# Kernel tuning notes

Hardware: AMD Instinct MI355X
Metric: run time of the kernel (lower is better)

## Reference

```python
import jax, jax.numpy as jnp
import numpy as np

NUM_HEAD = 16


def setup_inputs() -> dict:
    key = jax.random.key(0)
    k1, k2, k3 = jax.random.split(key, 3)
    E = 1024
    x = jax.random.normal(k1, (4, 2048, E), dtype=jnp.float32)
    W1 = jax.random.normal(k2, (E, 3 * E), dtype=jnp.float32) * 0.02
    b1 = jnp.zeros((3 * E,), dtype=jnp.float32)
    W2 = jax.random.normal(k3, (E, E), dtype=jnp.float32) * 0.02
    b2 = jnp.zeros((E,), dtype=jnp.float32)
    return {"x": x, "W1": W1, "b1": b1, "W2": W2, "b2": b2}


def reference(x, W1, b1, W2, b2):
    # Fused QKV projection: (n, s, 3E)
    h = x @ W1 + b1
    n, s, _ = h.shape
    # Split into heads FIRST (matches torch reshape), then transpose: (n, H, s, 3*d_head)
    h = h.reshape(n, s, NUM_HEAD, -1).transpose(0, 2, 1, 3)
    # Chunk last dim into q, k, v: each (n, H, s, d_head)
    q, k, v = jnp.split(h, 3, axis=-1)
    dk = jnp.asarray(v.shape[-1], x.dtype) ** 0.5
    # Naive full S x S attention (faithful to source)
    w = jnp.einsum("nhqd,nhkd->nhqk", q, k) / dk
    w = jax.nn.softmax(w, axis=-1)  # dropout1 is identity at eval
    att = jnp.einsum("nhqk,nhkd->nhqd", w, v)
    att = att.transpose(0, 2, 1, 3).reshape(n, s, -1)  # (n, s, E)
    return att @ W2 + b2  # dropout2 identity at eval
```

## Files before the change

### kernel.cpp

```cpp
#include <hip/hip_runtime.h>
#include <math.h>
#include <stdint.h>
#include <stddef.h>


#define SEQ    2048
#define NB     4
#define E_DIM  1024
#define N1     3072
#define M_TOK  8192
#define NHEAD  16
#define DHEAD  64

typedef __attribute__((ext_vector_type(4))) float    floatx4;
typedef __attribute__((ext_vector_type(8))) short    shortx8;
typedef __attribute__((ext_vector_type(4))) unsigned short ushortx4;

#if __has_builtin(__builtin_amdgcn_exp2f)
#define EXP2(x) __builtin_amdgcn_exp2f(x)
#else
#define EXP2(x) __expf((x) * 0.6931471805599453f)
#endif

__device__ __forceinline__ unsigned short f2bf(float f) {
    union { float f; unsigned u; } v; v.f = f;
    unsigned r = (v.u + 0x7FFFu + ((v.u >> 16) & 1u)) >> 16;
    return (unsigned short)r;
}
__device__ __forceinline__ unsigned fbits(float f) {
    union { float f; unsigned u; } v; v.f = f; return v.u;
}
__device__ __forceinline__ float bitsf(unsigned u) {
    union { unsigned u; float f; } v; v.u = u; return v.f;
}

__device__ __forceinline__ void gl_lds16(const void* g, void* l) {
    __builtin_amdgcn_global_load_lds(
        (const __attribute__((address_space(1))) unsigned int*)g,
        (__attribute__((address_space(3))) unsigned int*)l, 16, 0, 0);
}

__global__ __launch_bounds__(256) void cvt_bf16(
    const float* __restrict__ in, unsigned short* __restrict__ out)
{
    const size_t i = ((size_t)blockIdx.x * 256 + threadIdx.x) * 8;
    float4 a = *(const float4*)(in + i);
    float4 b = *(const float4*)(in + i + 4);
    ushortx4 o0 = { f2bf(a.x), f2bf(a.y), f2bf(a.z), f2bf(a.w) };
    ushortx4 o1 = { f2bf(b.x), f2bf(b.y), f2bf(b.z), f2bf(b.w) };
    *(ushortx4*)(out + i)     = o0;
    *(ushortx4*)(out + i + 4) = o1;
}

__global__ __launch_bounds__(256) void cvt_transpose(
    const float* __restrict__ W, unsigned short* __restrict__ Wt, int K, int N)
{
    __shared__ unsigned short tile[32][33];
    const int tx = threadIdx.x, ty = threadIdx.y;
    const int n0 = blockIdx.x * 32, k0 = blockIdx.y * 32;
#pragma unroll
    for (int r = 0; r < 4; ++r) {
        const int k = ty + r * 8;
        tile[tx][k] = f2bf(W[(size_t)(k0 + k) * N + n0 + tx]);
    }
    __syncthreads();
#pragma unroll
    for (int r = 0; r < 4; ++r) {
        const int n = ty + r * 8;
        Wt[(size_t)(n0 + n) * K + k0 + tx] = tile[n][tx];
    }
}

template <bool OUT_BF16, bool FUSE>
__global__ __launch_bounds__(256) void gemm_bf16(
    const short* __restrict__ A, const short* __restrict__ Bt,
    const float* __restrict__ bias, void* __restrict__ Cout,
    unsigned short* __restrict__ Vt,
    int M, int N, int K)
{
    __shared__ short As[128 * 32];
    __shared__ short Bs[128 * 32];

    const int t    = threadIdx.x;
    const int lane = t & 63, w = t >> 6;
    const int quad = lane >> 4, l15 = lane & 15;
    const int bm = blockIdx.y * 128, bn = blockIdx.x * 128;
    const int m0w = (w >> 1) * 64, n0w = (w & 1) * 64;

    const int lrow = lane >> 2;
    const int lcol = (lane & 3) * 8;
    const short* Ag0 = A  + (size_t)(bm + (2 * w + 0) * 16 + lrow) * K + lcol;
    const short* Ag1 = A  + (size_t)(bm + (2 * w + 1) * 16 + lrow) * K + lcol;
    const short* Bg0 = Bt + (size_t)(bn + (2 * w + 0) * 16 + lrow) * K + lcol;
    const short* Bg1 = Bt + (size_t)(bn + (2 * w + 1) * 16 + lrow) * K + lcol;
    short* Al0 = As + (2 * w + 0) * 512;
    short* Al1 = As + (2 * w + 1) * 512;
    short* Bl0 = Bs + (2 * w + 0) * 512;
    short* Bl1 = Bs + (2 * w + 1) * 512;

    floatx4 acc[4][4];
#pragma unroll
    for (int i = 0; i < 4; ++i)
#pragma unroll
        for (int j = 0; j < 4; ++j) acc[i][j] = (floatx4)0.f;

    for (int k0 = 0; k0 < K; k0 += 32) {
        __syncthreads();
        gl_lds16(Ag0, Al0); gl_lds16(Ag1, Al1);
        gl_lds16(Bg0, Bl0); gl_lds16(Bg1, Bl1);
        Ag0 += 32; Ag1 += 32; Bg0 += 32; Bg1 += 32;
        __syncthreads();

        shortx8 af[4], bf[4];
#pragma unroll
        for (int mi = 0; mi < 4; ++mi)
            af[mi] = *(const shortx8*)(As + (m0w + mi * 16 + l15) * 32 + quad * 8);
#pragma unroll
        for (int ni = 0; ni < 4; ++ni)
            bf[ni] = *(const shortx8*)(Bs + (n0w + ni * 16 + l15) * 32 + quad * 8);
#pragma unroll
        for (int mi = 0; mi < 4; ++mi)
#pragma unroll
            for (int ni = 0; ni < 4; ++ni)
                acc[mi][ni] = __builtin_amdgcn_mfma_f32_16x16x32_bf16(
                    af[mi], bf[ni], acc[mi][ni], 0, 0, 0);
    }

    float bv[4];
#pragma unroll
    for (int ni = 0; ni < 4; ++ni) bv[ni] = bias[bn + n0w + ni * 16 + l15];

#pragma unroll
    for (int ni = 0; ni < 4; ++ni) {
        const int col   = bn + n0w + ni * 16 + l15;
        const int cm    = col % 192;
        const int vhead = col / 192;
#pragma unroll
        for (int mi = 0; mi < 4; ++mi) {
            const int row0 = bm + m0w + mi * 16 + quad * 4;
            float v[4];
#pragma unroll
            for (int r = 0; r < 4; ++r) v[r] = acc[mi][ni][r] + bv[ni];
            if (OUT_BF16) {
                if (FUSE && cm < DHEAD) {
#pragma unroll
                    for (int r = 0; r < 4; ++r) v[r] *= 0.18033688011112042f;
                }
                unsigned short* H = (unsigned short*)Cout;
#pragma unroll
                for (int r = 0; r < 4; ++r)
                    H[(size_t)(row0 + r) * N + col] = f2bf(v[r]);
                if (FUSE && cm >= 2 * DHEAD) {
                    const int nb = row0 >> 11;
                    const int s  = row0 & 2047;
                    const int d  = cm - 2 * DHEAD;
                    ushortx4 pk = { f2bf(v[0]), f2bf(v[1]), f2bf(v[2]), f2bf(v[3]) };
                    *(ushortx4*)(Vt + ((size_t)(nb * NHEAD + vhead) * DHEAD + d) * SEQ + s) = pk;
                }
            } else {
                float* C = (float*)Cout;
#pragma unroll
                for (int r = 0; r < 4; ++r)
                    C[(size_t)(row0 + r) * N + col] = v[r];
            }
        }
    }
}

__global__ __launch_bounds__(256, 4) void attn_mfma(
    const short* __restrict__ h, const short* __restrict__ Vt,
    unsigned short* __restrict__ att)
{
    __shared__ short Ks[64 * 64];
    __shared__ short Vs[64 * 64];
    __shared__ short Pl[2][64 * 64];
    __shared__ float Ls2[2][2][64];

    const int t    = threadIdx.x;
    const int lane = t & 63, w = t >> 6;
    const int p    = w >> 1, e = w & 1;
    const int quad = lane >> 4, l15 = lane & 15;
    const int r7   = l15 & 7;
    const int bh = blockIdx.x, n = bh >> 4, head = bh & 15;
    const int q0 = blockIdx.y * 128 + p * 64;

    const short* hQ  = h + (size_t)n * SEQ * N1 + head * (3 * DHEAD);
    const short* hK  = hQ + DHEAD;
    const short* Vtb = Vt + (size_t)bh * DHEAD * SEQ;

    const int srow = t >> 2;
    const int sc0  = (t & 3) * 2;
    const int sk   = srow & 7;
    const short* gK = hK  + (size_t)srow * N1  + sc0 * 8;
    const short* gV = Vtb + (size_t)srow * SEQ + sc0 * 8;
    short* lK0 = Ks + srow * 64 + ((sc0    ) ^ sk) * 8;
    short* lK1 = Ks + srow * 64 + ((sc0 + 1) ^ sk) * 8;
    short* lV0 = Vs + srow * 64 + ((sc0    ) ^ sk) * 8;
    short* lV1 = Vs + srow * 64 + ((sc0 + 1) ^ sk) * 8;

    shortx8 qf[4][2];
#pragma unroll
    for (int qt = 0; qt < 4; ++qt)
#pragma unroll
        for (int kt = 0; kt < 2; ++kt)
            qf[qt][kt] = *(const shortx8*)(hQ + (size_t)(q0 + qt * 16 + l15) * N1
                                           + kt * 32 + quad * 8);

    floatx4 O[4][2];
    float lsum[4];
#pragma unroll
    for (int mi = 0; mi < 4; ++mi) {
        lsum[mi] = 0.f;
#pragma unroll
        for (int nt = 0; nt < 2; ++nt) O[mi][nt] = (floatx4)0.f;
    }

    int4 ka = *(const int4*)gK, kb = *(const int4*)(gK + 8);
    int4 va = *(const int4*)gV, vb = *(const int4*)(gV + 8);

    short* Pp = Pl[p];

    for (int kv0 = 0; kv0 < SEQ; kv0 += 64) {
        __syncthreads();
        *(int4*)lK0 = ka;
        *(int4*)lK1 = kb;
        *(int4*)lV0 = va;
        *(int4*)lV1 = vb;
        __syncthreads();
        if (kv0 + 64 < SEQ) {
            const short* gKn = gK + (size_t)(kv0 + 64) * N1;
            const short* gVn = gV + (kv0 + 64);
            ka = *(const int4*)gKn; kb = *(const int4*)(gKn + 8);
            va = *(const int4*)gVn; vb = *(const int4*)(gVn + 8);
        }

#pragma unroll
        for (int ii = 0; ii < 2; ++ii) {
            const int si = 2 * e + ii;
            const short* krow = Ks + (si * 16 + l15) * 64;
            shortx8 kf0 = *(const shortx8*)(krow + ((quad ^ r7) * 8));
            shortx8 kf1 = *(const shortx8*)(krow + (((quad ^ 4) ^ r7) * 8));
            floatx4 s[4];
#pragma unroll
            for (int qt = 0; qt < 4; ++qt) {
                s[qt] = __builtin_amdgcn_mfma_f32_16x16x32_bf16(
                    kf0, qf[qt][0], (floatx4)0.f, 0, 0, 0);
                s[qt] = __builtin_amdgcn_mfma_f32_16x16x32_bf16(
                    kf1, qf[qt][1], s[qt], 0, 0, 0);
            }
#pragma unroll
            for (int qt = 0; qt < 4; ++qt) {
                const float p0 = EXP2(s[qt][0]);
                const float p1 = EXP2(s[qt][1]);
                const float p2 = EXP2(s[qt][2]);
                const float p3 = EXP2(s[qt][3]);
                const unsigned d01 = __builtin_amdgcn_perm(fbits(p1), fbits(p0), 0x07060302u);
                const unsigned d23 = __builtin_amdgcn_perm(fbits(p3), fbits(p2), 0x07060302u);
                lsum[qt] += bitsf(d01 << 16) + bitsf(d01 & 0xFFFF0000u)
                          + bitsf(d23 << 16) + bitsf(d23 & 0xFFFF0000u);
                uint2 pk = { d01, d23 };
                *(uint2*)(Pp + (qt * 16 + l15) * 64
                          + ((si * 2 + (quad >> 1)) ^ r7) * 8 + (quad & 1) * 4) = pk;
            }
        }
        __syncthreads();

#pragma unroll
        for (int kt2 = 0; kt2 < 2; ++kt2) {
            const int coff = ((kt2 * 4 + quad) ^ r7) * 8;
            shortx8 pf[4], vf[2];
#pragma unroll
            for (int mi = 0; mi < 4; ++mi)
                pf[mi] = *(const shortx8*)(Pp + (mi * 16 + l15) * 64 + coff);
#pragma unroll
            for (int nt = 0; nt < 2; ++nt)
                vf[nt] = *(const shortx8*)(Vs + ((2 * e + nt) * 16 + l15) * 64 + coff);
#pragma unroll
            for (int mi = 0; mi < 4; ++mi)
#pragma unroll
                for (int nt = 0; nt < 2; ++nt)
                    O[mi][nt] = __builtin_amdgcn_mfma_f32_16x16x32_bf16(
                        pf[mi], vf[nt], O[mi][nt], 0, 0, 0);
        }
    }

#pragma unroll
    for (int qt = 0; qt < 4; ++qt) {
        lsum[qt] += __shfl_xor(lsum[qt], 16);
        lsum[qt] += __shfl_xor(lsum[qt], 32);
    }
    if (quad == 0) {
#pragma unroll
        for (int qt = 0; qt < 4; ++qt) Ls2[p][e][qt * 16 + l15] = lsum[qt];
    }
    __syncthreads();

#pragma unroll
    for (int mi = 0; mi < 4; ++mi)
#pragma unroll
        for (int r = 0; r < 4; ++r) {
            const int   ql  = mi * 16 + quad * 4 + r;
            const float inv = 1.f / (Ls2[p][0][ql] + Ls2[p][1][ql]);
            const size_t row = (size_t)n * SEQ + q0 + ql;
#pragma unroll
            for (int nt = 0; nt < 2; ++nt)
                att[row * E_DIM + head * DHEAD + (2 * e + nt) * 16 + l15] =
                    f2bf(O[mi][nt][r] * inv);
        }
}

extern "C" void kernel_launch(void* const* d_in, const int* in_sizes, int n_in,
                              void* d_out, int out_size, void* d_ws, size_t ws_size,
                              hipStream_t stream)
{
    const float* x  = (const float*)d_in[0];
    const float* W1 = (const float*)d_in[1];
    const float* b1 = (const float*)d_in[2];
    const float* W2 = (const float*)d_in[3];
    const float* b2 = (const float*)d_in[4];
    float* out = (float*)d_out;

    char* ws = (char*)d_ws;
    unsigned short* x_bf  = (unsigned short*)(ws);
    unsigned short* W1t   = (unsigned short*)(ws + (16u << 20));
    unsigned short* W2t   = (unsigned short*)(ws + (22u << 20));
    unsigned short* h_bf  = (unsigned short*)(ws + (24u << 20));
    unsigned short* attb  = (unsigned short*)(ws + (72u << 20));
    unsigned short* Vtw   = (unsigned short*)(ws + (88u << 20));

    cvt_bf16<<<dim3((M_TOK * E_DIM) / (256 * 8)), 256, 0, stream>>>(x, x_bf);
    cvt_transpose<<<dim3(N1 / 32, E_DIM / 32), dim3(32, 8), 0, stream>>>(W1, W1t, E_DIM, N1);
    cvt_transpose<<<dim3(E_DIM / 32, E_DIM / 32), dim3(32, 8), 0, stream>>>(W2, W2t, E_DIM, E_DIM);

    gemm_bf16<true, true><<<dim3(N1 / 128, M_TOK / 128), 256, 0, stream>>>(
        (const short*)x_bf, (const short*)W1t, b1, h_bf, Vtw, M_TOK, N1, E_DIM);

    attn_mfma<<<dim3(NB * NHEAD, SEQ / 128), 256, 0, stream>>>(
        (const short*)h_bf, (const short*)Vtw, attb);

    gemm_bf16<false, false><<<dim3(E_DIM / 128, M_TOK / 128), 256, 0, stream>>>(
        (const short*)attb, (const short*)W2t, b2, out, nullptr, M_TOK, E_DIM, E_DIM);
}
```

Baseline: 298.2 us.

## Keep attention probabilities in registers and double-buffer K/V tiles

Restructures the attention kernel so each wave owns 32 query rows and feeds the exponentiated scores straight from MFMA output registers into a 16x16x16 MFMA against V. This removes the P round-trip through shared memory and one barrier per tile. The row sums come from an extra MFMA with a ones vector instead of scalar adds and a cross-wave LDS reduction. K/V tiles are double-buffered in LDS so only one barrier per iteration remains, at the cost of more LDS and more, smaller MFMAs.

```diff
diff --git a/kernel.cpp b/kernel.cpp
--- a/kernel.cpp
+++ b/kernel.cpp
@@ -14,6 +14,7 @@
 
 typedef __attribute__((ext_vector_type(4))) float    floatx4;
 typedef __attribute__((ext_vector_type(8))) short    shortx8;
+typedef __attribute__((ext_vector_type(4))) short    shortx4;
 typedef __attribute__((ext_vector_type(4))) unsigned short ushortx4;
 
 #if __has_builtin(__builtin_amdgcn_exp2f)
@@ -22,6 +23,9 @@
 #define EXP2(x) __expf((x) * 0.6931471805599453f)
 #endif
 
+#define MFMA_K16(a, b, c) \
+    __builtin_amdgcn_mfma_f32_16x16x16bf16_1k((a), (b), (c), 0, 0, 0)
+
 __device__ __forceinline__ unsigned short f2bf(float f) {
     union { float f; unsigned u; } v; v.f = f;
     unsigned r = (v.u + 0x7FFFu + ((v.u >> 16) & 1u)) >> 16;
@@ -29,9 +33,6 @@
 }
 __device__ __forceinline__ unsigned fbits(float f) {
     union { float f; unsigned u; } v; v.f = f; return v.u;
-}
-__device__ __forceinline__ float bitsf(unsigned u) {
-    union { unsigned u; float f; } v; v.u = u; return v.f;
 }
 
 __device__ __forceinline__ void gl_lds16(const void* g, void* l) {
@@ -171,18 +172,15 @@
     const short* __restrict__ h, const short* __restrict__ Vt,
     unsigned short* __restrict__ att)
 {
-    __shared__ short Ks[64 * 64];
-    __shared__ short Vs[64 * 64];
-    __shared__ short Pl[2][64 * 64];
-    __shared__ float Ls2[2][2][64];
+    __shared__ short Ks[2][64 * 64];
+    __shared__ short Vs[2][64 * 64];
 
     const int t    = threadIdx.x;
     const int lane = t & 63, w = t >> 6;
-    const int p    = w >> 1, e = w & 1;
     const int quad = lane >> 4, l15 = lane & 15;
     const int r7   = l15 & 7;
     const int bh = blockIdx.x, n = bh >> 4, head = bh & 15;
-    const int q0 = blockIdx.y * 128 + p * 64;
+    const int q0 = blockIdx.y * 128 + w * 32;
 
     const short* hQ  = h + (size_t)n * SEQ * N1 + head * (3 * DHEAD);
     const short* hK  = hQ + DHEAD;
@@ -193,119 +191,105 @@
     const int sk   = srow & 7;
     const short* gK = hK  + (size_t)srow * N1  + sc0 * 8;
     const short* gV = Vtb + (size_t)srow * SEQ + sc0 * 8;
-    short* lK0 = Ks + srow * 64 + ((sc0    ) ^ sk) * 8;
-    short* lK1 = Ks + srow * 64 + ((sc0 + 1) ^ sk) * 8;
-    short* lV0 = Vs + srow * 64 + ((sc0    ) ^ sk) * 8;
-    short* lV1 = Vs + srow * 64 + ((sc0 + 1) ^ sk) * 8;
-
-    shortx8 qf[4][2];
-#pragma unroll
-    for (int qt = 0; qt < 4; ++qt)
+    const int oL0 = srow * 64 + ((sc0    ) ^ sk) * 8;
+    const int oL1 = srow * 64 + ((sc0 + 1) ^ sk) * 8;
+
+    shortx8 qf[2][2];
+#pragma unroll
+    for (int qt = 0; qt < 2; ++qt)
 #pragma unroll
         for (int kt = 0; kt < 2; ++kt)
             qf[qt][kt] = *(const shortx8*)(hQ + (size_t)(q0 + qt * 16 + l15) * N1
                                            + kt * 32 + quad * 8);
 
-    floatx4 O[4][2];
-    float lsum[4];
-#pragma unroll
-    for (int mi = 0; mi < 4; ++mi) {
-        lsum[mi] = 0.f;
-#pragma unroll
-        for (int nt = 0; nt < 2; ++nt) O[mi][nt] = (floatx4)0.f;
-    }
+    floatx4 O[2][4];
+    floatx4 Osum[2];
+#pragma unroll
+    for (int qt = 0; qt < 2; ++qt) {
+        Osum[qt] = (floatx4)0.f;
+#pragma unroll
+        for (int dt = 0; dt < 4; ++dt) O[qt][dt] = (floatx4)0.f;
+    }
+
+    const shortx4 ones = { (short)0x3F80, (short)0x3F80, (short)0x3F80, (short)0x3F80 };
+
+    const int NT = SEQ / 64;
 
     int4 ka = *(const int4*)gK, kb = *(const int4*)(gK + 8);
     int4 va = *(const int4*)gV, vb = *(const int4*)(gV + 8);
-
-    short* Pp = Pl[p];
-
-    for (int kv0 = 0; kv0 < SEQ; kv0 += 64) {
+    *(int4*)(&Ks[0][oL0]) = ka; *(int4*)(&Ks[0][oL1]) = kb;
+    *(int4*)(&Vs[0][oL0]) = va; *(int4*)(&Vs[0][oL1]) = vb;
+    gK += (size_t)64 * N1; gV += 64;
+
+    for (int it = 0; it < NT; ++it) {
+        const int buf = it & 1;
         __syncthreads();
-        *(int4*)lK0 = ka;
-        *(int4*)lK1 = kb;
-        *(int4*)lV0 = va;
-        *(int4*)lV1 = vb;
-        __syncthreads();
-        if (kv0 + 64 < SEQ) {
-            const short* gKn = gK + (size_t)(kv0 + 64) * N1;
-            const short* gVn = gV + (kv0 + 64);
-            ka = *(const int4*)gKn; kb = *(const int4*)(gKn + 8);
-            va = *(const int4*)gVn; vb = *(const int4*)(gVn + 8);
-        }
-
-#pragma unroll
-        for (int ii = 0; ii < 2; ++ii) {
-            const int si = 2 * e + ii;
-            const short* krow = Ks + (si * 16 + l15) * 64;
+
+        const bool more = (it + 1 < NT);
+        if (more) {
+            ka = *(const int4*)gK; kb = *(const int4*)(gK + 8);
+            va = *(const int4*)gV; vb = *(const int4*)(gV + 8);
+            gK += (size_t)64 * N1; gV += 64;
+        }
+
+        const short* Kb = &Ks[buf][0];
+        const short* Vb = &Vs[buf][0];
+
+#pragma unroll
+        for (int sl = 0; sl < 4; ++sl) {
+            const short* krow = Kb + (sl * 16 + l15) * 64;
             shortx8 kf0 = *(const shortx8*)(krow + ((quad ^ r7) * 8));
             shortx8 kf1 = *(const shortx8*)(krow + (((quad ^ 4) ^ r7) * 8));
-            floatx4 s[4];
-#pragma unroll
-            for (int qt = 0; qt < 4; ++qt) {
-                s[qt] = __builtin_amdgcn_mfma_f32_16x16x32_bf16(
+            shortx4 vf[4];
+#pragma unroll
+            for (int dt = 0; dt < 4; ++dt)
+                vf[dt] = *(const shortx4*)(Vb + (dt * 16 + l15) * 64
+                                           + (((sl * 4 + quad) ^ (r7 << 1)) << 2));
+
+            shortx4 pa[2];
+#pragma unroll
+            for (int qt = 0; qt < 2; ++qt) {
+                floatx4 s = __builtin_amdgcn_mfma_f32_16x16x32_bf16(
                     kf0, qf[qt][0], (floatx4)0.f, 0, 0, 0);
-                s[qt] = __builtin_amdgcn_mfma_f32_16x16x32_bf16(
-                    kf1, qf[qt][1], s[qt], 0, 0, 0);
+                s = __builtin_amdgcn_mfma_f32_16x16x32_bf16(
+                    kf1, qf[qt][1], s, 0, 0, 0);
+                const float p0 = EXP2(s[0]);
+                const float p1 = EXP2(s[1]);
+                const float p2 = EXP2(s[2]);
+                const float p3 = EXP2(s[3]);
+                union { uint2 u; shortx4 v; } cv;
+                cv.u.x = __builtin_amdgcn_perm(fbits(p1), fbits(p0), 0x07060302u);
+                cv.u.y = __builtin_amdgcn_perm(fbits(p3), fbits(p2), 0x07060302u);
+                pa[qt] = cv.v;
             }
-#pragma unroll
-            for (int qt = 0; qt < 4; ++qt) {
-                const float p0 = EXP2(s[qt][0]);
-                const float p1 = EXP2(s[qt][1]);
-                const float p2 = EXP2(s[qt][2]);
-                const float p3 = EXP2(s[qt][3]);
-                const unsigned d01 = __builtin_amdgcn_perm(fbits(p1), fbits(p0), 0x07060302u);
-                const unsigned d23 = __builtin_amdgcn_perm(fbits(p3), fbits(p2), 0x07060302u);
-                lsum[qt] += bitsf(d01 << 16) + bitsf(d01 & 0xFFFF0000u)
-                          + bitsf(d23 << 16) + bitsf(d23 & 0xFFFF0000u);
-                uint2 pk = { d01, d23 };
-                *(uint2*)(Pp + (qt * 16 + l15) * 64
-                          + ((si * 2 + (quad >> 1)) ^ r7) * 8 + (quad & 1) * 4) = pk;
+
+#pragma unroll
+            for (int qt = 0; qt < 2; ++qt) {
+                Osum[qt] = MFMA_K16(pa[qt], ones, Osum[qt]);
+#pragma unroll
+                for (int dt = 0; dt < 4; ++dt)
+                    O[qt][dt] = MFMA_K16(pa[qt], vf[dt], O[qt][dt]);
             }
         }
-        __syncthreads();
-
-#pragma unroll
-        for (int kt2 = 0; kt2 < 2; ++kt2) {
-            const int coff = ((kt2 * 4 + quad) ^ r7) * 8;
-            shortx8 pf[4], vf[2];
-#pragma unroll
-            for (int mi = 0; mi < 4; ++mi)
-                pf[mi] = *(const shortx8*)(Pp + (mi * 16 + l15) * 64 + coff);
-#pragma unroll
-            for (int nt = 0; nt < 2; ++nt)
-                vf[nt] = *(const shortx8*)(Vs + ((2 * e + nt) * 16 + l15) * 64 + coff);
-#pragma unroll
-            for (int mi = 0; mi < 4; ++mi)
-#pragma unroll
-                for (int nt = 0; nt < 2; ++nt)
-                    O[mi][nt] = __builtin_amdgcn_mfma_f32_16x16x32_bf16(
-                        pf[mi], vf[nt], O[mi][nt], 0, 0, 0);
-        }
-    }
-
-#pragma unroll
-    for (int qt = 0; qt < 4; ++qt) {
-        lsum[qt] += __shfl_xor(lsum[qt], 16);
-        lsum[qt] += __shfl_xor(lsum[qt], 32);
-    }
-    if (quad == 0) {
-#pragma unroll
-        for (int qt = 0; qt < 4; ++qt) Ls2[p][e][qt * 16 + l15] = lsum[qt];
-    }
-    __syncthreads();
-
-#pragma unroll
-    for (int mi = 0; mi < 4; ++mi)
+
+        if (more) {
+            short* Kn = &Ks[buf ^ 1][0];
+            short* Vn = &Vs[buf ^ 1][0];
+            *(int4*)(Kn + oL0) = ka; *(int4*)(Kn + oL1) = kb;
+            *(int4*)(Vn + oL0) = va; *(int4*)(Vn + oL1) = vb;
+        }
+    }
+
+    const size_t obase = ((size_t)n * SEQ + q0) * E_DIM + head * DHEAD;
+#pragma unroll
+    for (int qt = 0; qt < 2; ++qt)
 #pragma unroll
         for (int r = 0; r < 4; ++r) {
-            const int   ql  = mi * 16 + quad * 4 + r;
-            const float inv = 1.f / (Ls2[p][0][ql] + Ls2[p][1][ql]);
-            const size_t row = (size_t)n * SEQ + q0 + ql;
-#pragma unroll
-            for (int nt = 0; nt < 2; ++nt)
-                att[row * E_DIM + head * DHEAD + (2 * e + nt) * 16 + l15] =
-                    f2bf(O[mi][nt][r] * inv);
+            const float inv = 1.f / Osum[qt][r];
+            const size_t row = obase + (size_t)(qt * 16 + quad * 4 + r) * E_DIM;
+#pragma unroll
+            for (int dt = 0; dt < 4; ++dt)
+                att[row + dt * 16 + l15] = f2bf(O[qt][dt][r] * inv);
         }
 }
 
```

After: 283.8 us. -4.9%, faster.
